# Kernel tuning notes

Measured on AMD Instinct MI355X. Metric: run time of the kernel, lower is better.

The kernel has to match this reference:

```python
import jax, jax.numpy as jnp
import numpy as np


def setup_inputs() -> dict:
    key = jax.random.key(0)
    k1, k2, k3, k4 = jax.random.split(key, 4)
    T, B, D_in, D_out = 512, 128, 512, 512
    X = jax.random.normal(k1, (T, B, D_in), dtype=jnp.float32)
    # torch nn.Linear default init: U(-1/sqrt(fan_in), 1/sqrt(fan_in))
    lim_in = 1.0 / np.sqrt(D_in)
    lim_h = 1.0 / np.sqrt(D_out)
    W_in = jax.random.uniform(k2, (D_out, D_in), jnp.float32, -lim_in, lim_in)
    W_h = jax.random.uniform(k3, (D_out, D_out), jnp.float32, -lim_h, lim_h)
    b_h = jax.random.uniform(k4, (D_out,), jnp.float32, -lim_h, lim_h)
    return {"X": X, "W_in": W_in, "W_h": W_h, "b_h": b_h}


def reference(X, W_in, W_h, b_h):
    # X: [T, B, D_in]. h_{t+1} = sigmoid(x_t @ W_in^T + h_t @ W_h^T + b_h)
    B = X.shape[1]
    D_out = W_h.shape[0]
    # Precompute all input projections in one big GEMM (same math).
    Xproj = jnp.einsum('tbi,oi->tbo', X, W_in)  # [T, B, D_out]
    h0 = jnp.zeros((B, D_out), dtype=X.dtype)

    def step(h, xp):
        h_new = jax.nn.sigmoid(xp + h @ W_h.T + b_h)
        return h_new, None

    h_last, _ = jax.lax.scan(step, h0, Xproj)
    return h_last
```

## Files before the change

kernel.cpp:

```cpp
#include <hip/hip_runtime.h>
#include <hip/hip_bf16.h>
#include <stdint.h>

typedef _Float16 f16;
typedef _Float16 f16x2 __attribute__((ext_vector_type(2)));
typedef _Float16 f16x4 __attribute__((ext_vector_type(4)));
typedef _Float16 f16x8 __attribute__((ext_vector_type(8)));
typedef float f32x4 __attribute__((ext_vector_type(4)));
typedef int   i32x4 __attribute__((ext_vector_type(4)));

#define T_STEPS 512
#define BATCH   128
#define DD      512
#define LOG2E   1.44269504088896f

#define XP_OFF  0
#define WF_OFF  (67108864)
#define WHQ_OFF (67108864 + 524288)
#define SC_OFF  (67108864 + 524288 + 262144)

__device__ __forceinline__ f16x2 pk(float a, float b) {
    return __builtin_bit_cast(f16x2, __builtin_amdgcn_cvt_pkrtz(a, b));
}

__device__ __forceinline__ float fast_exp2(float x) {
#if __has_builtin(__builtin_amdgcn_exp2f)
    return __builtin_amdgcn_exp2f(x);
#else
    return exp2f(x);
#endif
}

__device__ __forceinline__ float fast_rcp(float x) {
#if __has_builtin(__builtin_amdgcn_rcpf)
    return __builtin_amdgcn_rcpf(x);
#else
    return 1.0f / x;
#endif
}

__device__ __forceinline__ uint32_t pack_u8(float s, int pos, uint32_t old) {
#if __has_builtin(__builtin_amdgcn_cvt_pk_u8_f32)
    return __builtin_amdgcn_cvt_pk_u8_f32(s, pos, old);
#else
    return old | (((uint32_t)(int)s & 0xFF) << (8 * pos));
#endif
}

#define GLDS(g, l) __builtin_amdgcn_global_load_lds(                               \
        (const __attribute__((address_space(1))) void*)(g),                        \
        (__attribute__((address_space(3))) void*)(l), 16, 0, 0)

__global__ __launch_bounds__(256) void prep_kernel(
        const float* __restrict__ Win, f16* __restrict__ Wf) {
    int idx = blockIdx.x * 256 + threadIdx.x;
    if (idx < 262144) Wf[idx] = (f16)Win[idx];
}

__global__ __launch_bounds__(64) void quant_kernel(
        const float* __restrict__ Wh, char* __restrict__ Whq, float* __restrict__ scales) {
    const int o = blockIdx.x, t = threadIdx.x;
    const float* row = Wh + (size_t)o * 512;
    float v[8];
    float m = 0.f;
#pragma unroll
    for (int j = 0; j < 8; j++) { v[j] = row[t * 8 + j]; m = fmaxf(m, fabsf(v[j])); }
#pragma unroll
    for (int off = 32; off > 0; off >>= 1) m = fmaxf(m, __shfl_xor(m, off));
    if (t == 0) scales[o] = -LOG2E * m * (1.0f / (127.0f * 127.0f));
    const float inv = 127.0f / m;
    const int rt = o >> 4, rl = o & 15;
    const int k0 = t * 8;
    const int ks = k0 >> 6, qq = (k0 >> 4) & 3, j0 = k0 & 15;
    const int l = qq * 16 + rl;
    char* dst = Whq + ((size_t)((rt * 8 + ks) * 64 + l)) * 16 + j0;
#pragma unroll
    for (int j = 0; j < 8; j++) dst[j] = (char)rintf(v[j] * inv);
}

__global__ __launch_bounds__(512, 4) void gemm_kernel(
        const float* __restrict__ X, const f16* __restrict__ Wf,
        const float* __restrict__ bias, f16* __restrict__ Xp) {
    const int tid = threadIdx.x;
    const int l = tid & 63, w = tid >> 6;
    const int q = l >> 4, rl = l & 15;
    const int wm = w >> 2, wn = w & 3;
    const int blk = blockIdx.x;
    const int xcd = blk & 7, kk = blk >> 3;
    const int m_blk = (xcd * 64 + (kk >> 1)) * 128;
    const int n_blk = (kk & 1) * 256;

    __shared__ __align__(16) float As[2][128 * 32];
    __shared__ __align__(16) f16   Bs[2][256 * 32];

    const float* aSrc[2];
#pragma unroll
    for (int c = 0; c < 2; c++)
        aSrc[c] = X + (size_t)(m_blk + w * 16 + c * 8 + (l >> 3)) * 512
                    + (((l & 7) ^ (l >> 3)) << 2);
    const f16* bSrc[2];
#pragma unroll
    for (int c = 0; c < 2; c++)
        bSrc[c] = Wf + (size_t)(n_blk + w * 32 + c * 16 + (l >> 2)) * 512
                     + (((l & 3) ^ ((l >> 3) & 3)) << 3);

    f32x4 acc[4][4] = {};
    const int swA0 = (((2 * q)     ^ (rl & 7)) << 2);
    const int swA1 = (((2 * q + 1) ^ (rl & 7)) << 2);
    const int swB  = ((q ^ ((rl >> 1) & 3)) << 3);

#pragma unroll
    for (int c = 0; c < 2; c++) GLDS(aSrc[c], &As[0][(w * 16 + c * 8) * 32]);
#pragma unroll
    for (int c = 0; c < 2; c++) GLDS(bSrc[c], &Bs[0][(w * 32 + c * 16) * 32]);

    for (int t = 0; t < 16; ++t) {
        const int cur = t & 1;
        __syncthreads();
        if (t < 15) {
            const int kf = (t + 1) * 32;
#pragma unroll
            for (int c = 0; c < 2; c++) GLDS(aSrc[c] + kf, &As[cur ^ 1][(w * 16 + c * 8) * 32]);
#pragma unroll
            for (int c = 0; c < 2; c++) GLDS(bSrc[c] + kf, &Bs[cur ^ 1][(w * 32 + c * 16) * 32]);
        }
        f16x8 af4[4], bf4[4];
#pragma unroll
        for (int i = 0; i < 4; i++) {
            const int row = wm * 64 + i * 16 + rl;
            const float4 h0 = *(const float4*)&As[cur][row * 32 + swA0];
            const float4 h1 = *(const float4*)&As[cur][row * 32 + swA1];
            f16x2 p0 = pk(h0.x, h0.y), p1 = pk(h0.z, h0.w);
            f16x2 p2 = pk(h1.x, h1.y), p3 = pk(h1.z, h1.w);
            f16x8 tv;
            tv[0] = p0[0]; tv[1] = p0[1]; tv[2] = p1[0]; tv[3] = p1[1];
            tv[4] = p2[0]; tv[5] = p2[1]; tv[6] = p3[0]; tv[7] = p3[1];
            af4[i] = tv;
        }
#pragma unroll
        for (int j = 0; j < 4; j++) {
            const int row = wn * 64 + j * 16 + rl;
            bf4[j] = *(const f16x8*)&Bs[cur][row * 32 + swB];
        }
#pragma unroll
        for (int i = 0; i < 4; i++)
#pragma unroll
            for (int j = 0; j < 4; j++)
                acc[i][j] = __builtin_amdgcn_mfma_f32_16x16x32_f16(bf4[j], af4[i], acc[i][j], 0, 0, 0);
    }
#pragma unroll
    for (int j = 0; j < 4; j++) {
        const float4 b4 = *(const float4*)&bias[n_blk + wn * 64 + j * 16 + q * 4];
        const float bb[4] = {b4.x, b4.y, b4.z, b4.w};
#pragma unroll
        for (int i = 0; i < 4; i++) {
            const int m = m_blk + wm * 64 + i * 16 + rl;
            f16x4 v;
#pragma unroll
            for (int r = 0; r < 4; r++)
                v[r] = (f16)(-LOG2E * (acc[i][j][r] + bb[r]));
            *(f16x4*)(Xp + (size_t)m * 512 + n_blk + wn * 64 + j * 16 + q * 4) = v;
        }
    }
}

__global__ __launch_bounds__(1024) void rnn_kernel(
        const char* __restrict__ Whq, const float* __restrict__ scales,
        const f16* __restrict__ Xp, float* __restrict__ out) {
    const int wg = blockIdx.x;
    const int tid = threadIdx.x;
    const int l = tid & 63, w = tid >> 6;
    const int bl = l & 15;
    const int q = l >> 4;
    const int b = wg * 16 + bl;

    __shared__ __align__(16) uint32_t hT[2][2048];

    i32x4 af[2][8];
    {
        const i32x4* wp = (const i32x4*)Whq;
#pragma unroll
        for (int mt = 0; mt < 2; mt++)
#pragma unroll
            for (int ks = 0; ks < 8; ks++)
                af[mt][ks] = wp[((w * 2 + mt) * 8 + ks) * 64 + l];
    }
    float sc[2][4];
#pragma unroll
    for (int mt = 0; mt < 2; mt++)
#pragma unroll
        for (int r = 0; r < 4; r++)
            sc[mt][r] = scales[w * 32 + mt * 16 + q * 4 + r];

    for (int i = tid; i < 2048; i += 1024) hT[0][i] = 0u;
    __syncthreads();

    const f16* xpb = Xp + (size_t)b * 512 + w * 32 + q * 4;
    f16x4 xn0 = *(const f16x4*)(xpb);
    f16x4 xn1 = *(const f16x4*)(xpb + 16);

    const float K127 = 1.0f / 127.0f;
    for (int t = 0; t < T_STEPS; t++) {
        f16x4 xc0 = xn0, xc1 = xn1;
        const size_t tn = (size_t)(t < T_STEPS - 1 ? t + 1 : t) * (BATCH * 512);
        xn0 = *(const f16x4*)(xpb + tn);
        xn1 = *(const f16x4*)(xpb + tn + 16);

        const int rb = t & 1;
        const uint32_t* hrow = &hT[rb][l * 4];
        uint32_t* hwr = &hT[1 - rb][w * 128 + bl * 4 + q];

        i32x4 acc0 = {};
        __builtin_amdgcn_s_setprio(1);
#pragma unroll
        for (int ks = 0; ks < 8; ks++) {
            i32x4 bfr = *(const i32x4*)(hrow + ks * 256);
            acc0 = __builtin_amdgcn_mfma_i32_16x16x64_i8(af[0][ks], bfr, acc0, 0, 0, 0);
        }
        __builtin_amdgcn_s_setprio(0);

        uint32_t pk0 = 0;
#pragma unroll
        for (int r = 0; r < 4; r++) {
            float tt = fmaf((float)acc0[r], sc[0][r], (float)xc0[r]);
            float e  = fast_exp2(tt);
            float eq = fmaf(e, K127, K127);
            float sg = fast_rcp(eq) + 0.5f;
            pk0 = pack_u8(sg, r, pk0);
        }
        hwr[0] = pk0;

        i32x4 acc1 = {};
        __builtin_amdgcn_s_setprio(1);
#pragma unroll
        for (int ks = 0; ks < 8; ks++) {
            i32x4 bfr = *(const i32x4*)(hrow + ks * 256);
            acc1 = __builtin_amdgcn_mfma_i32_16x16x64_i8(af[1][ks], bfr, acc1, 0, 0, 0);
        }
        __builtin_amdgcn_s_setprio(0);

        uint32_t pk1 = 0;
#pragma unroll
        for (int r = 0; r < 4; r++) {
            float tt = fmaf((float)acc1[r], sc[1][r], (float)xc1[r]);
            float e  = fast_exp2(tt);
            float eq = fmaf(e, K127, K127);
            float sg = fast_rcp(eq) + 0.5f;
            pk1 = pack_u8(sg, r, pk1);
        }
        hwr[64] = pk1;
        __syncthreads();
    }
#pragma unroll
    for (int mt = 0; mt < 2; mt++) {
        uint32_t pkq = hT[T_STEPS & 1][w * 128 + mt * 64 + bl * 4 + q];
        float4 o;
        o.x = (float)((pkq      ) & 0xFF) * K127;
        o.y = (float)((pkq >>  8) & 0xFF) * K127;
        o.z = (float)((pkq >> 16) & 0xFF) * K127;
        o.w = (float)((pkq >> 24) & 0xFF) * K127;
        *(float4*)(out + (size_t)b * 512 + w * 32 + mt * 16 + q * 4) = o;
    }
}

extern "C" void kernel_launch(void* const* d_in, const int* in_sizes, int n_in,
                              void* d_out, int out_size, void* d_ws, size_t ws_size,
                              hipStream_t stream) {
    const float* X   = (const float*)d_in[0];
    const float* Win = (const float*)d_in[1];
    const float* Wh  = (const float*)d_in[2];
    const float* bh  = (const float*)d_in[3];
    float* out = (float*)d_out;
    char* ws = (char*)d_ws;
    f16* Xp      = (f16*)(ws + XP_OFF);
    f16* Wf      = (f16*)(ws + WF_OFF);
    char* Whq    = (char*)(ws + WHQ_OFF);
    float* Sc    = (float*)(ws + SC_OFF);

    prep_kernel<<<1024, 256, 0, stream>>>(Win, Wf);
    quant_kernel<<<512, 64, 0, stream>>>(Wh, Whq, Sc);
    gemm_kernel<<<1024, 512, 0, stream>>>(X, Wf, bh, Xp);
    rnn_kernel<<<8, 1024, 0, stream>>>(Whq, Sc, Xp, out);
}
```

Baseline: 738.1 us.

## Shrink GEMM N-tile to 128 and reuse hidden-state fragments across both RNN MFMA chains

The input-projection GEMM now uses a 128x128 tile instead of 128x256, so it launches twice as many blocks, each with a smaller accumulator and B buffer. This raises parallelism and occupancy, but each block re-reads A more often relative to the work it does. In the recurrent kernel, the eight hidden-state LDS fragments are loaded once per step and shared by both output-tile MFMA chains instead of being loaded twice. Both chains and the first sigmoid now run under one high-priority section. This halves LDS reads on the serial critical path, at the cost of more live registers.

New measurement: 707.8 us. 4.1% less time.

```diff
diff --git a/kernel.cpp b/kernel.cpp
--- a/kernel.cpp
+++ b/kernel.cpp
@@ -86,33 +86,29 @@
     const int q = l >> 4, rl = l & 15;
     const int wm = w >> 2, wn = w & 3;
     const int blk = blockIdx.x;
-    const int xcd = blk & 7, kk = blk >> 3;
-    const int m_blk = (xcd * 64 + (kk >> 1)) * 128;
-    const int n_blk = (kk & 1) * 256;
+    const int xcd = blk & 7, idx = blk >> 3;
+    const int m_blk = (xcd * 64 + (idx >> 2)) * 128;
+    const int n_blk = (idx & 3) * 128;
 
     __shared__ __align__(16) float As[2][128 * 32];
-    __shared__ __align__(16) f16   Bs[2][256 * 32];
+    __shared__ __align__(16) f16   Bs[2][128 * 32];
 
     const float* aSrc[2];
 #pragma unroll
     for (int c = 0; c < 2; c++)
         aSrc[c] = X + (size_t)(m_blk + w * 16 + c * 8 + (l >> 3)) * 512
                     + (((l & 7) ^ (l >> 3)) << 2);
-    const f16* bSrc[2];
-#pragma unroll
-    for (int c = 0; c < 2; c++)
-        bSrc[c] = Wf + (size_t)(n_blk + w * 32 + c * 16 + (l >> 2)) * 512
-                     + (((l & 3) ^ ((l >> 3) & 3)) << 3);
-
-    f32x4 acc[4][4] = {};
+    const f16* bSrc = Wf + (size_t)(n_blk + w * 16 + (l >> 2)) * 512
+                         + (((l & 3) ^ ((l >> 3) & 3)) << 3);
+
+    f32x4 acc[4][2] = {};
     const int swA0 = (((2 * q)     ^ (rl & 7)) << 2);
     const int swA1 = (((2 * q + 1) ^ (rl & 7)) << 2);
     const int swB  = ((q ^ ((rl >> 1) & 3)) << 3);
 
 #pragma unroll
     for (int c = 0; c < 2; c++) GLDS(aSrc[c], &As[0][(w * 16 + c * 8) * 32]);
-#pragma unroll
-    for (int c = 0; c < 2; c++) GLDS(bSrc[c], &Bs[0][(w * 32 + c * 16) * 32]);
+    GLDS(bSrc, &Bs[0][(w * 16) * 32]);
 
     for (int t = 0; t < 16; ++t) {
         const int cur = t & 1;
@@ -121,10 +117,9 @@
             const int kf = (t + 1) * 32;
 #pragma unroll
             for (int c = 0; c < 2; c++) GLDS(aSrc[c] + kf, &As[cur ^ 1][(w * 16 + c * 8) * 32]);
-#pragma unroll
-            for (int c = 0; c < 2; c++) GLDS(bSrc[c] + kf, &Bs[cur ^ 1][(w * 32 + c * 16) * 32]);
-        }
-        f16x8 af4[4], bf4[4];
+            GLDS(bSrc + kf, &Bs[cur ^ 1][(w * 16) * 32]);
+        }
+        f16x8 af4[4], bf4[2];
 #pragma unroll
         for (int i = 0; i < 4; i++) {
             const int row = wm * 64 + i * 16 + rl;
@@ -138,19 +133,19 @@
             af4[i] = tv;
         }
 #pragma unroll
-        for (int j = 0; j < 4; j++) {
-            const int row = wn * 64 + j * 16 + rl;
+        for (int j = 0; j < 2; j++) {
+            const int row = wn * 32 + j * 16 + rl;
             bf4[j] = *(const f16x8*)&Bs[cur][row * 32 + swB];
         }
 #pragma unroll
         for (int i = 0; i < 4; i++)
 #pragma unroll
-            for (int j = 0; j < 4; j++)
+            for (int j = 0; j < 2; j++)
                 acc[i][j] = __builtin_amdgcn_mfma_f32_16x16x32_f16(bf4[j], af4[i], acc[i][j], 0, 0, 0);
     }
 #pragma unroll
-    for (int j = 0; j < 4; j++) {
-        const float4 b4 = *(const float4*)&bias[n_blk + wn * 64 + j * 16 + q * 4];
+    for (int j = 0; j < 2; j++) {
+        const float4 b4 = *(const float4*)&bias[n_blk + wn * 32 + j * 16 + q * 4];
         const float bb[4] = {b4.x, b4.y, b4.z, b4.w};
 #pragma unroll
         for (int i = 0; i < 4; i++) {
@@ -159,7 +154,7 @@
 #pragma unroll
             for (int r = 0; r < 4; r++)
                 v[r] = (f16)(-LOG2E * (acc[i][j][r] + bb[r]));
-            *(f16x4*)(Xp + (size_t)m * 512 + n_blk + wn * 64 + j * 16 + q * 4) = v;
+            *(f16x4*)(Xp + (size_t)m * 512 + n_blk + wn * 32 + j * 16 + q * 4) = v;
         }
     }
 }
@@ -210,14 +205,16 @@
         const uint32_t* hrow = &hT[rb][l * 4];
         uint32_t* hwr = &hT[1 - rb][w * 128 + bl * 4 + q];
 
-        i32x4 acc0 = {};
+        i32x4 bfr[8];
+#pragma unroll
+        for (int ks = 0; ks < 8; ks++)
+            bfr[ks] = *(const i32x4*)(hrow + ks * 256);
+
+        i32x4 acc0 = {}, acc1 = {};
         __builtin_amdgcn_s_setprio(1);
 #pragma unroll
-        for (int ks = 0; ks < 8; ks++) {
-            i32x4 bfr = *(const i32x4*)(hrow + ks * 256);
-            acc0 = __builtin_amdgcn_mfma_i32_16x16x64_i8(af[0][ks], bfr, acc0, 0, 0, 0);
-        }
-        __builtin_amdgcn_s_setprio(0);
+        for (int ks = 0; ks < 8; ks++)
+            acc0 = __builtin_amdgcn_mfma_i32_16x16x64_i8(af[0][ks], bfr[ks], acc0, 0, 0, 0);
 
         uint32_t pk0 = 0;
 #pragma unroll
@@ -230,13 +227,9 @@
         }
         hwr[0] = pk0;
 
-        i32x4 acc1 = {};
-        __builtin_amdgcn_s_setprio(1);
-#pragma unroll
-        for (int ks = 0; ks < 8; ks++) {
-            i32x4 bfr = *(const i32x4*)(hrow + ks * 256);
-            acc1 = __builtin_amdgcn_mfma_i32_16x16x64_i8(af[1][ks], bfr, acc1, 0, 0, 0);
-        }
+#pragma unroll
+        for (int ks = 0; ks < 8; ks++)
+            acc1 = __builtin_amdgcn_mfma_i32_16x16x64_i8(af[1][ks], bfr[ks], acc1, 0, 0, 0);
         __builtin_amdgcn_s_setprio(0);
 
         uint32_t pk1 = 0;
@@ -279,6 +272,6 @@
 
     prep_kernel<<<1024, 256, 0, stream>>>(Win, Wf);
     quant_kernel<<<512, 64, 0, stream>>>(Wh, Whq, Sc);
-    gemm_kernel<<<1024, 512, 0, stream>>>(X, Wf, bh, Xp);
+    gemm_kernel<<<2048, 512, 0, stream>>>(X, Wf, bh, Xp);
     rnn_kernel<<<8, 1024, 0, stream>>>(Whq, Sc, Xp, out);
 }
```
